# Optimization experiments

Hardware: AMD Instinct MI355X
Metric: run time of the kernel (lower is better)

The kernel has to match this reference:

```python
import jax, jax.numpy as jnp
import numpy as np

NEG_SLOPE = 0.01  # torch LeakyReLU default

def leaky_relu(x):
    return jnp.where(x >= 0, x, NEG_SLOPE * x)

def setup_inputs() -> dict:
    key = jax.random.key(0)
    ks = jax.random.split(key, 12)
    D = 128
    N_U, N_I, E = 100000, 50000, 1000000
    s = 1.0 / np.sqrt(D)
    return {
        "h_user": jax.random.normal(ks[0], (N_U, D), jnp.float32),
        "h_item": jax.random.normal(ks[1], (N_I, D), jnp.float32),
        "src_idx": jax.random.randint(ks[2], (E,), 0, N_U, jnp.int64) if jax.config.jax_enable_x64 else jax.random.randint(ks[2], (E,), 0, N_U, jnp.int32),
        "dst_idx": jax.random.randint(ks[3], (E,), 0, N_I, jnp.int32),
        "W_left": jax.random.normal(ks[4], (D, D), jnp.float32) * s,
        "b_left": jax.random.normal(ks[5], (D,), jnp.float32) * s,
        "W_right": jax.random.normal(ks[6], (D, D), jnp.float32) * s,
        "b_right": jax.random.normal(ks[7], (D,), jnp.float32) * s,
        "W1": jax.random.normal(ks[8], (D, D), jnp.float32) * s,
        "b1": jax.random.normal(ks[9], (D,), jnp.float32) * s,
        "W2": jax.random.normal(ks[10], (D, 1), jnp.float32) * s,
        "b2": jax.random.normal(ks[11], (1,), jnp.float32) * s,
    }

def reference(h_user, h_item, src_idx, dst_idx,
              W_left, b_left, W_right, b_right, W1, b1, W2, b2):
    # node linear transforms (dropout is identity in eval mode)
    u_f = h_user @ W_left + b_left      # [N_u, D]
    i_f = h_item @ W_right + b_right    # [N_i, D]
    # edge gather + add (dgl fn.u_add_v)
    score = u_f[src_idx] + i_f[dst_idx]  # [E, D]
    # pred MLP: LeakyReLU -> Linear(D,D) -> LeakyReLU -> Linear(D,1) -> LeakyReLU
    x = leaky_relu(score)
    x = leaky_relu(x @ W1 + b1)
    x = leaky_relu(x @ W2 + b2)         # [E, 1]
    return x
```

## Files before the change

kernel.cpp:

```cpp
#include <hip/hip_runtime.h>

typedef __attribute__((ext_vector_type(8))) short bf16x8;
typedef __attribute__((ext_vector_type(4))) float f32x4;
typedef __attribute__((ext_vector_type(2))) float f32x2;

__device__ __forceinline__ float leaky(float v) { return fmaxf(v, 0.01f * v); }

__device__ __forceinline__ unsigned short f2bf(float a) {
    unsigned int u = __float_as_uint(a);
    return (unsigned short)((u + 0x7FFFu + ((u >> 16) & 1u)) >> 16);
}

__device__ __forceinline__ unsigned int cvtpk(float a, float b) {
#if __has_builtin(__builtin_amdgcn_cvt_pk_bf16_f32)
    typedef __attribute__((ext_vector_type(2))) __bf16 bf2_t;
    bf2_t v = __builtin_amdgcn_cvt_pk_bf16_f32(a, b);
    return __builtin_bit_cast(unsigned int, v);
#else
    unsigned int ua = __float_as_uint(a);
    ua = (ua + 0x7FFFu + ((ua >> 16) & 1u)) >> 16;
    unsigned int ub = __float_as_uint(b);
    ub = (ub + 0x7FFFu + ((ub >> 16) & 1u)) >> 16;
    return ua | (ub << 16);
#endif
}

__device__ __forceinline__ f32x2 unpk2(unsigned int d) {
    f32x2 r;
    r.x = __uint_as_float(d << 16);
    r.y = __uint_as_float(d & 0xFFFF0000u);
    return r;
}

__device__ __forceinline__ unsigned int mix1(unsigned int u, unsigned int i) {
    f32x2 v = unpk2(u) + unpk2(i);
    v = __builtin_elementwise_max(v, v * 0.01f);
    return cvtpk(v.x, v.y);
}

__global__ __launch_bounds__(128) void prep(const float* __restrict__ WL,
                                            const float* __restrict__ WR,
                                            const float* __restrict__ W1,
                                            unsigned short* __restrict__ WLf,
                                            unsigned short* __restrict__ WRf,
                                            unsigned short* __restrict__ Wf) {
    int g = blockIdx.x;
    int f = (g & 127) * 128 + threadIdx.x;
    int j = f & 7, lane = (f >> 3) & 63, nt = (f >> 9) & 7, kb = f >> 12;
    int n = nt * 16 + (lane & 15);
    int kf = kb * 32 + (lane >> 4) * 8 + j;
    if (g < 128) {
        WLf[f] = f2bf(WL[kf * 128 + n]);
    } else if (g < 256) {
        WRf[f] = f2bf(WR[kf * 128 + n]);
    } else {
        int k = (kf & 7) * 16 + (kf >> 3);
        Wf[f] = f2bf(W1[k * 128 + n]);
    }
}

#define PITCH 136

__global__ __launch_bounds__(512, 8) void node_mfma2(const float* __restrict__ h_user,
                                                     const float* __restrict__ h_item,
                                                     const unsigned short* __restrict__ WLf,
                                                     const unsigned short* __restrict__ WRf,
                                                     const float* __restrict__ b_left,
                                                     const float* __restrict__ b_right,
                                                     unsigned short* __restrict__ u_f,
                                                     unsigned short* __restrict__ i_f,
                                                     int N_U, int N_I, int BU) {
    bool isU = (int)blockIdx.x < BU;
    const float* h = isU ? h_user : h_item;
    const unsigned short* Wfr = isU ? WLf : WRf;
    const float* b = isU ? b_left : b_right;
    unsigned short* out = isU ? u_f : i_f;
    int N = isU ? N_U : N_I;
    int r0 = (isU ? blockIdx.x : blockIdx.x - BU) * 128;

    __shared__ unsigned short xt[128 * PITCH];
    int t = threadIdx.x;
    int s = t & 31;
    int el0 = t >> 5;

    f32x4 g[8];
#pragma unroll
    for (int pass = 0; pass < 8; ++pass) {
        int row = min(r0 + pass * 16 + el0, N - 1);
        g[pass] = *(const f32x4*)(h + (size_t)row * 128 + s * 4);
    }
#pragma unroll
    for (int pass = 0; pass < 8; ++pass) {
        int el = pass * 16 + el0;
        unsigned int* rp = (unsigned int*)(xt + el * PITCH + s * 4);
        rp[0] = cvtpk(g[pass].x, g[pass].y);
        rp[1] = cvtpk(g[pass].z, g[pass].w);
    }
    __syncthreads();

    int wave = t >> 6;
    int lane = t & 63;
    int col = lane & 15;
    int quad = lane >> 4;
    int wp = wave >> 1;
    int ch = wave & 1;
    int m0 = wp * 32;

    f32x4 acc[2][4];
#pragma unroll
    for (int mt = 0; mt < 2; ++mt)
#pragma unroll
        for (int i = 0; i < 4; ++i) acc[mt][i] = (f32x4){0.f, 0.f, 0.f, 0.f};

#pragma unroll
    for (int kb = 0; kb < 4; ++kb) {
        bf16x8 afr[2];
#pragma unroll
        for (int mt = 0; mt < 2; ++mt)
            afr[mt] = *(const bf16x8*)(xt + (m0 + mt * 16 + col) * PITCH + kb * 32 + quad * 8);
#pragma unroll
        for (int i = 0; i < 4; ++i) {
            int nt = ch * 4 + i;
            bf16x8 bfr = *(const bf16x8*)(Wfr + ((kb * 8 + nt) * 64 + lane) * 8);
            acc[0][i] = __builtin_amdgcn_mfma_f32_16x16x32_bf16(afr[0], bfr, acc[0][i], 0, 0, 0);
            acc[1][i] = __builtin_amdgcn_mfma_f32_16x16x32_bf16(afr[1], bfr, acc[1][i], 0, 0, 0);
        }
    }

    float bb[4];
#pragma unroll
    for (int i = 0; i < 4; ++i) bb[i] = b[(ch * 4 + i) * 16 + col];
#pragma unroll
    for (int mt = 0; mt < 2; ++mt)
#pragma unroll
        for (int rr = 0; rr < 4; ++rr) {
            int row = r0 + m0 + mt * 16 + quad * 4 + rr;
            uint2 v;
            v.x = cvtpk(acc[mt][0][rr] + bb[0], acc[mt][1][rr] + bb[1]);
            v.y = cvtpk(acc[mt][2][rr] + bb[2], acc[mt][3][rr] + bb[3]);
            if (row < N) *(uint2*)(out + (size_t)row * 128 + col * 8 + ch * 4) = v;
        }
}

#define TE 128

__global__ __launch_bounds__(512, 6) void edge_kernel(
    const unsigned short* __restrict__ u_f, const unsigned short* __restrict__ i_f,
    const int* __restrict__ src, const int* __restrict__ dst,
    const unsigned short* __restrict__ Wf,
    const float* __restrict__ b1, const float* __restrict__ W2,
    const float* __restrict__ b2, float* __restrict__ out, int E) {
    __shared__ unsigned short xt[TE * PITCH];
    __shared__ float zb[4][2][32];
    int t = threadIdx.x;
    int e0 = blockIdx.x * TE;

    int s = t & 15;
    int el0 = t >> 4;

    int su[4], sd[4];
#pragma unroll
    for (int pass = 0; pass < 4; ++pass) {
        int ec = min(e0 + pass * 32 + el0, E - 1);
        su[pass] = src[ec];
        sd[pass] = dst[ec];
    }
    uint4 ug[4], ig[4];
#pragma unroll
    for (int pass = 0; pass < 4; ++pass) {
        ug[pass] = *(const uint4*)(u_f + (size_t)su[pass] * 128 + s * 8);
        ig[pass] = *(const uint4*)(i_f + (size_t)sd[pass] * 128 + s * 8);
    }
#pragma unroll
    for (int pass = 0; pass < 4; ++pass) {
        uint4 a;
        a.x = mix1(ug[pass].x, ig[pass].x);
        a.y = mix1(ug[pass].y, ig[pass].y);
        a.z = mix1(ug[pass].z, ig[pass].z);
        a.w = mix1(ug[pass].w, ig[pass].w);
        *(uint4*)(xt + (pass * 32 + el0) * PITCH + s * 8) = a;
    }
    __syncthreads();

    int wave = t >> 6;
    int lane = t & 63;
    int col = lane & 15;
    int quad = lane >> 4;
    int wp = wave >> 1;
    int ch = wave & 1;
    int m0 = wp * 32;

    f32x4 acc[2][4];
#pragma unroll
    for (int mt = 0; mt < 2; ++mt)
#pragma unroll
        for (int i = 0; i < 4; ++i) acc[mt][i] = (f32x4){0.f, 0.f, 0.f, 0.f};

#pragma unroll
    for (int kb = 0; kb < 4; ++kb) {
        bf16x8 afr[2];
#pragma unroll
        for (int mt = 0; mt < 2; ++mt)
            afr[mt] = *(const bf16x8*)(xt + (m0 + mt * 16 + col) * PITCH + kb * 32 + quad * 8);
#pragma unroll
        for (int i = 0; i < 4; ++i) {
            int nt = ch * 4 + i;
            bf16x8 bfr = *(const bf16x8*)(Wf + ((kb * 8 + nt) * 64 + lane) * 8);
            acc[0][i] = __builtin_amdgcn_mfma_f32_16x16x32_bf16(afr[0], bfr, acc[0][i], 0, 0, 0);
            acc[1][i] = __builtin_amdgcn_mfma_f32_16x16x32_bf16(afr[1], bfr, acc[1][i], 0, 0, 0);
        }
    }

    f32x4 p[2];
#pragma unroll
    for (int mt = 0; mt < 2; ++mt) p[mt] = (f32x4){0.f, 0.f, 0.f, 0.f};

#pragma unroll
    for (int i = 0; i < 4; ++i) {
        int n = (ch * 4 + i) * 16 + col;
        float bb = b1[n];
        float ww = W2[n];
#pragma unroll
        for (int mt = 0; mt < 2; ++mt) {
            f32x4 y = acc[mt][i] + bb;
            y = __builtin_elementwise_max(y, y * 0.01f);
            p[mt] += y * ww;
        }
    }
#pragma unroll
    for (int off = 1; off < 16; off <<= 1)
#pragma unroll
        for (int mt = 0; mt < 2; ++mt)
#pragma unroll
            for (int rr = 0; rr < 4; ++rr) p[mt][rr] += __shfl_xor(p[mt][rr], off, 64);

    if (col == 0) {
#pragma unroll
        for (int mt = 0; mt < 2; ++mt)
#pragma unroll
            for (int rr = 0; rr < 4; ++rr)
                zb[wp][ch][mt * 16 + quad * 4 + rr] = p[mt][rr];
    }
    __syncthreads();

    if (t < 128) {
        int g = t >> 5;
        int idx = t & 31;
        float z = zb[g][0][idx] + zb[g][1][idx] + b2[0];
        int e = e0 + g * 32 + idx;
        if (e < E) out[e] = leaky(z);
    }
}

extern "C" void kernel_launch(void* const* d_in, const int* in_sizes, int n_in,
                              void* d_out, int out_size, void* d_ws, size_t ws_size,
                              hipStream_t stream) {
    const float* h_user  = (const float*)d_in[0];
    const float* h_item  = (const float*)d_in[1];
    const int*   src_idx = (const int*)d_in[2];
    const int*   dst_idx = (const int*)d_in[3];
    const float* W_left  = (const float*)d_in[4];
    const float* b_left  = (const float*)d_in[5];
    const float* W_right = (const float*)d_in[6];
    const float* b_right = (const float*)d_in[7];
    const float* W1      = (const float*)d_in[8];
    const float* b1      = (const float*)d_in[9];
    const float* W2      = (const float*)d_in[10];
    const float* b2      = (const float*)d_in[11];
    float* out = (float*)d_out;

    int N_U = in_sizes[0] / 128;
    int N_I = in_sizes[1] / 128;
    int E   = in_sizes[2];

    unsigned short* Wf  = (unsigned short*)d_ws;
    unsigned short* WLf = Wf + 16384;
    unsigned short* WRf = WLf + 16384;
    unsigned short* u_f = (unsigned short*)((char*)d_ws + 131072);
    unsigned short* i_f = u_f + (size_t)N_U * 128;

    prep<<<384, 128, 0, stream>>>(W_left, W_right, W1, WLf, WRf, Wf);

    int BU = (N_U + 127) / 128;
    int BI = (N_I + 127) / 128;
    node_mfma2<<<BU + BI, 512, 0, stream>>>(h_user, h_item, WLf, WRf, b_left, b_right,
                                            u_f, i_f, N_U, N_I, BU);

    edge_kernel<<<(E + TE - 1) / TE, 512, 0, stream>>>(u_f, i_f, src_idx, dst_idx,
                                                       Wf, b1, W2, b2, out, E);
}
```

Before: 226.4 us.

## Stage node outputs through LDS for coalesced stores and split edge launch in three

The node kernel now writes its bf16 results into shared memory and then copies whole rows to global memory with 16-byte stores, replacing scattered 8-byte stores; its occupancy hint drops from 8 to 6. The edge kernel folds the b1 bias into the accumulator initialisation and hoists the bias and W2 loads ahead of the gather. The edge launch is split into three consecutive launches over block ranges using a block offset. The aim is to reduce write inefficiency and per-block overhead, but the extra launches add launch cost without any overlap, since all three run on the same stream.

```diff
diff --git a/kernel.cpp b/kernel.cpp
--- a/kernel.cpp
+++ b/kernel.cpp
@@ -61,7 +61,7 @@
 
 #define PITCH 136
 
-__global__ __launch_bounds__(512, 8) void node_mfma2(const float* __restrict__ h_user,
+__global__ __launch_bounds__(512, 6) void node_mfma2(const float* __restrict__ h_user,
                                                      const float* __restrict__ h_item,
                                                      const unsigned short* __restrict__ WLf,
                                                      const unsigned short* __restrict__ WRf,
@@ -78,7 +78,7 @@
     int N = isU ? N_U : N_I;
     int r0 = (isU ? blockIdx.x : blockIdx.x - BU) * 128;
 
-    __shared__ unsigned short xt[128 * PITCH];
+    __shared__ __attribute__((aligned(16))) unsigned short xt[128 * PITCH];
     int t = threadIdx.x;
     int s = t & 31;
     int el0 = t >> 5;
@@ -130,16 +130,31 @@
     float bb[4];
 #pragma unroll
     for (int i = 0; i < 4; ++i) bb[i] = b[(ch * 4 + i) * 16 + col];
+
+    __syncthreads();
+
 #pragma unroll
     for (int mt = 0; mt < 2; ++mt)
 #pragma unroll
         for (int rr = 0; rr < 4; ++rr) {
-            int row = r0 + m0 + mt * 16 + quad * 4 + rr;
+            int row = m0 + mt * 16 + quad * 4 + rr;
             uint2 v;
             v.x = cvtpk(acc[mt][0][rr] + bb[0], acc[mt][1][rr] + bb[1]);
             v.y = cvtpk(acc[mt][2][rr] + bb[2], acc[mt][3][rr] + bb[3]);
-            if (row < N) *(uint2*)(out + (size_t)row * 128 + col * 8 + ch * 4) = v;
-        }
+            *(uint2*)(xt + (size_t)row * 128 + col * 8 + ch * 4) = v;
+        }
+    __syncthreads();
+
+    {
+        int row = t >> 2;
+        int seg = t & 3;
+        if (r0 + row < N) {
+            const uint4* lp = (const uint4*)(xt + (size_t)row * 128 + seg * 32);
+            uint4* gp = (uint4*)(out + (size_t)(r0 + row) * 128 + seg * 32);
+            uint4 a0 = lp[0], a1 = lp[1], a2 = lp[2], a3 = lp[3];
+            gp[0] = a0; gp[1] = a1; gp[2] = a2; gp[3] = a3;
+        }
+    }
 }
 
 #define TE 128
@@ -149,38 +164,14 @@
     const int* __restrict__ src, const int* __restrict__ dst,
     const unsigned short* __restrict__ Wf,
     const float* __restrict__ b1, const float* __restrict__ W2,
-    const float* __restrict__ b2, float* __restrict__ out, int E) {
+    const float* __restrict__ b2, float* __restrict__ out, int E, int bofs) {
     __shared__ unsigned short xt[TE * PITCH];
     __shared__ float zb[4][2][32];
     int t = threadIdx.x;
-    int e0 = blockIdx.x * TE;
+    int e0 = (blockIdx.x + bofs) * TE;
 
     int s = t & 15;
     int el0 = t >> 4;
-
-    int su[4], sd[4];
-#pragma unroll
-    for (int pass = 0; pass < 4; ++pass) {
-        int ec = min(e0 + pass * 32 + el0, E - 1);
-        su[pass] = src[ec];
-        sd[pass] = dst[ec];
-    }
-    uint4 ug[4], ig[4];
-#pragma unroll
-    for (int pass = 0; pass < 4; ++pass) {
-        ug[pass] = *(const uint4*)(u_f + (size_t)su[pass] * 128 + s * 8);
-        ig[pass] = *(const uint4*)(i_f + (size_t)sd[pass] * 128 + s * 8);
-    }
-#pragma unroll
-    for (int pass = 0; pass < 4; ++pass) {
-        uint4 a;
-        a.x = mix1(ug[pass].x, ig[pass].x);
-        a.y = mix1(ug[pass].y, ig[pass].y);
-        a.z = mix1(ug[pass].z, ig[pass].z);
-        a.w = mix1(ug[pass].w, ig[pass].w);
-        *(uint4*)(xt + (pass * 32 + el0) * PITCH + s * 8) = a;
-    }
-    __syncthreads();
 
     int wave = t >> 6;
     int lane = t & 63;
@@ -190,11 +181,47 @@
     int ch = wave & 1;
     int m0 = wp * 32;
 
+    float bb[4], ww[4];
+#pragma unroll
+    for (int i = 0; i < 4; ++i) {
+        int n = (ch * 4 + i) * 16 + col;
+        bb[i] = b1[n];
+        ww[i] = W2[n];
+    }
+    float b2v = b2[0];
+
+    int su[4], sd[4];
+#pragma unroll
+    for (int pass = 0; pass < 4; ++pass) {
+        int ec = min(e0 + pass * 32 + el0, E - 1);
+        su[pass] = src[ec];
+        sd[pass] = dst[ec];
+    }
+    {
+        uint4 ug[4], ig[4];
+#pragma unroll
+        for (int pass = 0; pass < 4; ++pass) {
+            ug[pass] = *(const uint4*)(u_f + (size_t)su[pass] * 128 + s * 8);
+            ig[pass] = *(const uint4*)(i_f + (size_t)sd[pass] * 128 + s * 8);
+        }
+#pragma unroll
+        for (int pass = 0; pass < 4; ++pass) {
+            uint4 a;
+            a.x = mix1(ug[pass].x, ig[pass].x);
+            a.y = mix1(ug[pass].y, ig[pass].y);
+            a.z = mix1(ug[pass].z, ig[pass].z);
+            a.w = mix1(ug[pass].w, ig[pass].w);
+            *(uint4*)(xt + (pass * 32 + el0) * PITCH + s * 8) = a;
+        }
+    }
+    __syncthreads();
+
     f32x4 acc[2][4];
 #pragma unroll
     for (int mt = 0; mt < 2; ++mt)
 #pragma unroll
-        for (int i = 0; i < 4; ++i) acc[mt][i] = (f32x4){0.f, 0.f, 0.f, 0.f};
+        for (int i = 0; i < 4; ++i)
+            acc[mt][i] = (f32x4){bb[i], bb[i], bb[i], bb[i]};
 
 #pragma unroll
     for (int kb = 0; kb < 4; ++kb) {
@@ -211,20 +238,17 @@
         }
     }
 
-    f32x4 p[2];
-#pragma unroll
-    for (int mt = 0; mt < 2; ++mt) p[mt] = (f32x4){0.f, 0.f, 0.f, 0.f};
+    f32x4 pz[2];
+#pragma unroll
+    for (int mt = 0; mt < 2; ++mt) pz[mt] = (f32x4){0.f, 0.f, 0.f, 0.f};
 
 #pragma unroll
     for (int i = 0; i < 4; ++i) {
-        int n = (ch * 4 + i) * 16 + col;
-        float bb = b1[n];
-        float ww = W2[n];
 #pragma unroll
         for (int mt = 0; mt < 2; ++mt) {
-            f32x4 y = acc[mt][i] + bb;
+            f32x4 y = acc[mt][i];
             y = __builtin_elementwise_max(y, y * 0.01f);
-            p[mt] += y * ww;
+            pz[mt] += y * ww[i];
         }
     }
 #pragma unroll
@@ -232,21 +256,21 @@
 #pragma unroll
         for (int mt = 0; mt < 2; ++mt)
 #pragma unroll
-            for (int rr = 0; rr < 4; ++rr) p[mt][rr] += __shfl_xor(p[mt][rr], off, 64);
+            for (int rr = 0; rr < 4; ++rr) pz[mt][rr] += __shfl_xor(pz[mt][rr], off, 64);
 
     if (col == 0) {
 #pragma unroll
         for (int mt = 0; mt < 2; ++mt)
 #pragma unroll
             for (int rr = 0; rr < 4; ++rr)
-                zb[wp][ch][mt * 16 + quad * 4 + rr] = p[mt][rr];
+                zb[wp][ch][mt * 16 + quad * 4 + rr] = pz[mt][rr];
     }
     __syncthreads();
 
     if (t < 128) {
         int g = t >> 5;
         int idx = t & 31;
-        float z = zb[g][0][idx] + zb[g][1][idx] + b2[0];
+        float z = zb[g][0][idx] + zb[g][1][idx] + b2v;
         int e = e0 + g * 32 + idx;
         if (e < E) out[e] = leaky(z);
     }
@@ -286,6 +310,14 @@
     node_mfma2<<<BU + BI, 512, 0, stream>>>(h_user, h_item, WLf, WRf, b_left, b_right,
                                             u_f, i_f, N_U, N_I, BU);
 
-    edge_kernel<<<(E + TE - 1) / TE, 512, 0, stream>>>(u_f, i_f, src_idx, dst_idx,
-                                                       Wf, b1, W2, b2, out, E);
-}
+    int NBLK = (E + TE - 1) / TE;
+    int C = (NBLK + 2) / 3;
+    for (int part = 0; part < 3; ++part) {
+        int bofs = part * C;
+        int nb = NBLK - bofs;
+        if (nb <= 0) break;
+        if (nb > C) nb = C;
+        edge_kernel<<<nb, 512, 0, stream>>>(u_f, i_f, src_idx, dst_idx,
+                                            Wf, b1, W2, b2, out, E, bofs);
+    }
+}
```

After: 245.5 us. +8.4%, slower.
